# Kernel tuning notes

Measured on AMD Instinct MI355X. Metric: run time of the kernel, lower is better.

## Reference

```python
import jax, jax.numpy as jnp
import numpy as np

B, T, E, H = 2, 2048, 1024, 16
HS = E // H  # head size = 64
EPS = 1e-5


def setup_inputs() -> dict:
    key = jax.random.key(0)
    ks = jax.random.split(key, 12)
    s_e = 1.0 / np.sqrt(E)
    s_4e = 1.0 / np.sqrt(4 * E)
    return {
        "x": jax.random.normal(ks[0], (B, T, E), dtype=jnp.float32),
        # per-head projections (no bias), stacked over heads: [H, E, HS]
        "Wq": jax.random.uniform(ks[1], (H, E, HS), jnp.float32, -s_e, s_e),
        "Wk": jax.random.uniform(ks[2], (H, E, HS), jnp.float32, -s_e, s_e),
        "Wv": jax.random.uniform(ks[3], (H, E, HS), jnp.float32, -s_e, s_e),
        # output projection
        "Wo": jax.random.uniform(ks[4], (E, E), jnp.float32, -s_e, s_e),
        "bo": jax.random.uniform(ks[5], (E,), jnp.float32, -s_e, s_e),
        # feed-forward
        "W1": jax.random.uniform(ks[6], (E, 4 * E), jnp.float32, -s_e, s_e),
        "b1": jax.random.uniform(ks[7], (4 * E,), jnp.float32, -s_e, s_e),
        "W2": jax.random.uniform(ks[8], (4 * E, E), jnp.float32, -s_4e, s_4e),
        "b2": jax.random.uniform(ks[9], (E,), jnp.float32, -s_4e, s_4e),
        # layernorms
        "g1": jnp.ones((E,), jnp.float32),
        "be1": jnp.zeros((E,), jnp.float32),
        "g2": jnp.ones((E,), jnp.float32),
        "be2": jnp.zeros((E,), jnp.float32),
    }


def _layernorm(x, g, b):
    mu = jnp.mean(x, axis=-1, keepdims=True)
    var = jnp.var(x, axis=-1, keepdims=True)
    return (x - mu) * jax.lax.rsqrt(var + EPS) * g + b


def reference(x, Wq, Wk, Wv, Wo, bo, W1, b1, W2, b2, g1, be1, g2, be2):
    Bx, Tx, Ex = x.shape
    # --- multi-head causal self-attention (dropout = identity in eval) ---
    q = jnp.einsum("bte,hed->bhtd", x, Wq)
    k = jnp.einsum("bte,hed->bhtd", x, Wk)
    v = jnp.einsum("bte,hed->bhtd", x, Wv)
    scale = HS ** -0.5
    scores = jnp.einsum("bhtd,bhsd->bhts", q, k) * scale  # [B,H,T,T]
    causal = jnp.tril(jnp.ones((Tx, Tx), dtype=bool))
    scores = jnp.where(causal, scores, -jnp.inf)
    att = jax.nn.softmax(scores, axis=-1)
    out = jnp.einsum("bhts,bhsd->bhtd", att, v)  # [B,H,T,HS]
    out = out.transpose(0, 2, 1, 3).reshape(Bx, Tx, Ex)  # concat heads
    out = out @ Wo + bo
    # --- residual + LN1 ---
    x = _layernorm(x + out, g1, be1)
    # --- feed-forward ---
    h = jax.nn.relu(x @ W1 + b1)
    ff = h @ W2 + b2
    # --- residual + LN2 ---
    return _layernorm(x + ff, g2, be2)
```

## Files before the change

### kernel.cpp

```cpp
#include <hip/hip_runtime.h>
#include <hip/hip_bf16.h>
#include <cstdint>
#include <cstddef>

typedef __hip_bfloat16 bf16;
typedef __attribute__((ext_vector_type(8))) short short8;
typedef __attribute__((ext_vector_type(4))) float f32x4;

#define B_  2
#define T_  2048
#define E_  1024
#define H_  16
#define HS_ 64
#define EPS_ 1e-5f
#define NEG_BIG -1.0e30f
#define SCL2E 0.18033688011112042f

__device__ __forceinline__ float b2f(bf16 v) { return __bfloat162float(v); }
__device__ __forceinline__ bf16  f2b(float v) { return __float2bfloat16(v); }
__device__ __forceinline__ ushort f2bs(float v) { bf16 b = __float2bfloat16(v); return *(ushort*)&b; }
__device__ __forceinline__ float ld1(const bf16* p) { return b2f(*p); }
__device__ __forceinline__ float ld1(const float* p) { return *p; }
__device__ __forceinline__ void st1(bf16* p, float v) { *p = f2b(v); }
__device__ __forceinline__ void st1(float* p, float v) { *p = v; }

__device__ __forceinline__ float fexp2(float x) {
#if __has_builtin(__builtin_amdgcn_exp2f)
    return __builtin_amdgcn_exp2f(x);
#else
    return exp2f(x);
#endif
}

__device__ __forceinline__ void gload16(const void* g, const void* l) {
    __builtin_amdgcn_global_load_lds(
        (const __attribute__((address_space(1))) unsigned int*)(size_t)g,
        (__attribute__((address_space(3))) unsigned int*)(unsigned int)(size_t)l,
        16, 0, 0);
}

__device__ __forceinline__ void transpose_tile_s(short t[64][72],
                                                 const float* in, size_t ldin,
                                                 bf16* out, size_t ldout,
                                                 int r0, int c0)
{
    const int tid = threadIdx.x;
    const int tr = tid >> 2, tc4 = (tid & 3) * 16;

    const float* p = in + (size_t)(r0 + tr) * ldin + c0 + tc4;
    float4 v0 = ((const float4*)p)[0], v1 = ((const float4*)p)[1];
    float4 v2 = ((const float4*)p)[2], v3 = ((const float4*)p)[3];
    union { ushort u[16]; uint4 q[2]; } pk;
    pk.u[0] = f2bs(v0.x); pk.u[1] = f2bs(v0.y); pk.u[2]  = f2bs(v0.z); pk.u[3]  = f2bs(v0.w);
    pk.u[4] = f2bs(v1.x); pk.u[5] = f2bs(v1.y); pk.u[6]  = f2bs(v1.z); pk.u[7]  = f2bs(v1.w);
    pk.u[8] = f2bs(v2.x); pk.u[9] = f2bs(v2.y); pk.u[10] = f2bs(v2.z); pk.u[11] = f2bs(v2.w);
    pk.u[12] = f2bs(v3.x); pk.u[13] = f2bs(v3.y); pk.u[14] = f2bs(v3.z); pk.u[15] = f2bs(v3.w);
    *(uint4*)&t[tr][tc4]     = pk.q[0];
    *(uint4*)&t[tr][tc4 + 8] = pk.q[1];
    __syncthreads();

    const int tcI = tid >> 2, rj = (tid & 3) * 16;
    union { ushort u[16]; uint4 q[2]; } po;
    #pragma unroll
    for (int j = 0; j < 16; j++) po.u[j] = (ushort)t[rj + j][tcI];
    bf16* op = out + (size_t)(c0 + tcI) * ldout + r0 + rj;
    ((uint4*)op)[0] = po.q[0];
    ((uint4*)op)[1] = po.q[1];
}

__global__ __launch_bounds__(256) void prep_kernel(const float* __restrict__ x,
                                                   ushort* __restrict__ xb,
                                                   const float* __restrict__ Wq,
                                                   const float* __restrict__ Wk,
                                                   const float* __restrict__ Wv,
                                                   bf16* __restrict__ WqkvT,
                                                   const float* __restrict__ Wo,
                                                   bf16* __restrict__ WoT)
{
    __shared__ short t[64][72];
    const int bid = blockIdx.x;
    if (bid < 2048) {
        int i = (bid * 256 + (int)threadIdx.x) * 8;
        float4 a = ((const float4*)(x + i))[0];
        float4 b = ((const float4*)(x + i))[1];
        union { ushort u[8]; uint4 v; } p;
        p.u[0] = f2bs(a.x); p.u[1] = f2bs(a.y); p.u[2] = f2bs(a.z); p.u[3] = f2bs(a.w);
        p.u[4] = f2bs(b.x); p.u[5] = f2bs(b.y); p.u[6] = f2bs(b.z); p.u[7] = f2bs(b.w);
        *(uint4*)(xb + i) = p.v;
    } else if (bid < 2048 + 768) {
        const int i = bid - 2048;
        const int s = i >> 4, xt = i & 15;
        const int proj = s >> 4, h = s & 15;
        const float* W = (proj == 0) ? Wq : ((proj == 1) ? Wk : Wv);
        transpose_tile_s(t, W + (size_t)h * E_ * HS_, HS_,
                         WqkvT + ((size_t)proj * E_ + h * 64) * E_, E_,
                         xt * 64, 0);
    } else {
        const int i = bid - 2816;
        transpose_tile_s(t, Wo, E_, WoT, E_, (i >> 4) * 64, (i & 15) * 64);
    }
}

__global__ __launch_bounds__(256) void prep2_kernel(const float* __restrict__ W1,
                                                    bf16* __restrict__ W1T,
                                                    const float* __restrict__ W2,
                                                    bf16* __restrict__ W2T)
{
    __shared__ short t[64][72];
    const int bid = blockIdx.x;
    if (bid < 1024) {
        transpose_tile_s(t, W1, 4 * E_, W1T, E_,
                         (bid & 15) * 64, (bid >> 4) * 64);
    } else {
        const int i = bid - 1024;
        transpose_tile_s(t, W2, E_, W2T, 4 * E_,
                         (i >> 4) * 64, (i & 15) * 64);
    }
}

__global__ __launch_bounds__(256) void vt_transpose(const bf16* __restrict__ qkv,
                                                    bf16* __restrict__ vT)
{
    __shared__ short t[64][72];
    const int tid = threadIdx.x;
    const int bh  = blockIdx.y;
    const int b   = bh >> 4, h = bh & 15;
    const int t0  = blockIdx.x * 64;

    const bf16* in = qkv + ((size_t)b * T_) * (3 * E_) + 2 * E_ + h * 64;
    const int tr = tid >> 2, tc4 = (tid & 3) * 16;
    const bf16* p = in + (size_t)(t0 + tr) * (3 * E_) + tc4;
    uint4 q0 = ((const uint4*)p)[0];
    uint4 q1 = ((const uint4*)p)[1];
    *(uint4*)&t[tr][tc4]     = q0;
    *(uint4*)&t[tr][tc4 + 8] = q1;
    __syncthreads();

    const int tcI = tid >> 2, rj = (tid & 3) * 16;
    union { ushort u[16]; uint4 q[2]; } po;
    #pragma unroll
    for (int j = 0; j < 16; j++) po.u[j] = (ushort)t[rj + j][tcI];
    bf16* op = vT + ((size_t)bh * 64 + tcI) * T_ + t0 + rj;
    ((uint4*)op)[0] = po.q[0];
    ((uint4*)op)[1] = po.q[1];
}

template <int WROWS, int WCOLS, int MF, int NF, int KS, bool BIAS, bool RELU,
          typename TO>
__global__ __launch_bounds__(256) void gemm_bt(const bf16* __restrict__ A,
                                               const bf16* __restrict__ BT,
                                               const float* __restrict__ bias,
                                               TO* __restrict__ C,
                                               int M, int N, int K)
{
    constexpr int BM = WROWS * MF * 16;
    constexpr int BN = WCOLS * NF * 16;
    __shared__ short Asm[KS][BM][32];
    __shared__ short Bsm[KS][BN][32];

    const int tid  = threadIdx.x;
    const int wv   = tid >> 6, lane = tid & 63;
    const int quad = lane >> 4, l16 = lane & 15;
    const int row0 = blockIdx.y * BM, col0 = blockIdx.x * BN;
    const int mr0  = (wv / WCOLS) * MF * 16;
    const int nc0  = (wv % WCOLS) * NF * 16;

    const int sr = tid >> 2, sc = tid & 3;
    const bf16* Ag = A  + (size_t)(row0 + sr) * K + sc * 8;
    const bf16* Bg = BT + (size_t)(col0 + (sr % BN)) * K + sc * 8;

    f32x4 acc[MF][NF];
    #pragma unroll
    for (int i = 0; i < MF; i++)
        #pragma unroll
        for (int j = 0; j < NF; j++) acc[i][j] = (f32x4){0.f, 0.f, 0.f, 0.f};

    for (int kt = 0; kt < K; kt += 32 * KS) {
        __syncthreads();
        #pragma unroll
        for (int g = 0; g < KS; g++) {
            #pragma unroll
            for (int l = 0; l < BM / 64; l++)
                gload16(Ag + g * 32 + (size_t)l * 64 * K, &Asm[g][l * 64 + wv * 16][0]);
            #pragma unroll
            for (int l = 0; l < BN / 64; l++)
                gload16(Bg + g * 32 + (size_t)l * 64 * K, &Bsm[g][l * 64 + wv * 16][0]);
        }
        Ag += 32 * KS; Bg += 32 * KS;
        __syncthreads();

        #pragma unroll
        for (int g = 0; g < KS; g++) {
            short8 af[MF], bfr[NF];
            #pragma unroll
            for (int mf = 0; mf < MF; mf++)
                af[mf] = *(const short8*)&Asm[g][mr0 + mf * 16 + l16][quad * 8];
            #pragma unroll
            for (int nf = 0; nf < NF; nf++)
                bfr[nf] = *(const short8*)&Bsm[g][nc0 + nf * 16 + l16][quad * 8];
            #pragma unroll
            for (int mf = 0; mf < MF; mf++)
                #pragma unroll
                for (int nf = 0; nf < NF; nf++)
                    acc[mf][nf] = __builtin_amdgcn_mfma_f32_16x16x32_bf16(
                        af[mf], bfr[nf], acc[mf][nf], 0, 0, 0);
        }
    }

    #pragma unroll
    for (int nf = 0; nf < NF; nf++) {
        const int col = col0 + nc0 + nf * 16 + l16;
        const float bv = BIAS ? bias[col] : 0.f;
        #pragma unroll
        for (int mf = 0; mf < MF; mf++) {
            #pragma unroll
            for (int r = 0; r < 4; r++) {
                const int row = row0 + mr0 + mf * 16 + quad * 4 + r;
                float v = acc[mf][nf][r] + bv;
                if (RELU) v = fmaxf(v, 0.f);
                st1(&C[(size_t)row * N + col], v);
            }
        }
    }
}

__global__ __launch_bounds__(256) void attn_mfma(const bf16* __restrict__ qkv,
                                                 const bf16* __restrict__ vT,
                                                 bf16* __restrict__ outp)
{
    __shared__ short Klds[128][72];
    __shared__ short Vlds[64][136];
    __shared__ short Plds[4][16][136];

    const int tid  = threadIdx.x;
    const int w    = tid >> 6, lane = tid & 63;
    const int quad = lane >> 4, l16 = lane & 15;

    const int p    = blockIdx.y * 32 + blockIdx.x;
    const int bh   = (p & 7) * 4 + ((p >> 3) & 3);
    const int tile = 31 - (p >> 5);
    const int b    = bh >> 4, h = bh & 15;
    const size_t rowb = (size_t)b * T_ * 3 * E_;
    const int t0    = tile * 64;
    const int qbase = t0 + w * 16;

    const int kkey = tid >> 1, kdh = (tid & 1) * 32;
    const bf16* Kg = qkv + rowb + E_ + h * HS_ + kdh;
    const int vd = tid >> 2, vseg = (tid & 3) * 32;
    const bf16* Vg = vT + ((size_t)bh * 64 + vd) * T_ + vseg;

    short8 vone;
    #pragma unroll
    for (int j = 0; j < 8; j++) vone[j] = (short)0x3F80;

    const bf16* Qp = qkv + rowb + (size_t)(qbase + l16) * (3 * E_) + h * HS_;
    const short8 aq0 = *(const short8*)(Qp + quad * 8);
    const short8 aq1 = *(const short8*)(Qp + 32 + quad * 8);

    f32x4 o[4], o4;
    #pragma unroll
    for (int f = 0; f < 4; f++) o[f] = (f32x4){0.f, 0.f, 0.f, 0.f};
    o4 = (f32x4){0.f, 0.f, 0.f, 0.f};
    float mrow = NEG_BIG;

    for (int kt0 = 0; kt0 <= t0; kt0 += 128) {
        __syncthreads();
        {
            const int kr = (kt0 + kkey < T_) ? kt0 + kkey : T_ - 1;
            const bf16* kp = Kg + (size_t)kr * (3 * E_);
            *(uint4*)&Klds[kkey][kdh]      = ((const uint4*)kp)[0];
            *(uint4*)&Klds[kkey][kdh + 8]  = ((const uint4*)kp)[1];
            *(uint4*)&Klds[kkey][kdh + 16] = ((const uint4*)kp)[2];
            *(uint4*)&Klds[kkey][kdh + 24] = ((const uint4*)kp)[3];
            const bf16* vp = Vg + kt0;
            *(uint4*)&Vlds[vd][vseg]       = ((const uint4*)vp)[0];
            *(uint4*)&Vlds[vd][vseg + 8]   = ((const uint4*)vp)[1];
            *(uint4*)&Vlds[vd][vseg + 16]  = ((const uint4*)vp)[2];
            *(uint4*)&Vlds[vd][vseg + 24]  = ((const uint4*)vp)[3];
        }
        __syncthreads();

        const bool active = (kt0 <= qbase + 15);
        const int nv0 = ((qbase + 15 - kt0) >> 4) + 1;
        const int nvalid = active ? (nv0 < 8 ? nv0 : 8) : 0;

        float ps[8][4];
        #pragma unroll
        for (int c = 0; c < 8; c++) {
            if (c < nvalid) {
                const int kc = kt0 + c * 16;
                const int krow = c * 16 + l16;
                short8 bk0 = *(const short8*)&Klds[krow][quad * 8];
                short8 bk1 = *(const short8*)&Klds[krow][32 + quad * 8];
                f32x4 s = (f32x4){0.f, 0.f, 0.f, 0.f};
                s = __builtin_amdgcn_mfma_f32_16x16x32_bf16(bk0, aq0, s, 0, 0, 0);
                s = __builtin_amdgcn_mfma_f32_16x16x32_bf16(bk1, aq1, s, 0, 0, 0);
                const bool needmask = (kc + 15 > qbase);
                #pragma unroll
                for (int r = 0; r < 4; r++) {
                    float sv = s[r] * SCL2E;
                    if (needmask && (kc + quad * 4 + r > qbase + l16)) sv = NEG_BIG;
                    ps[c][r] = sv;
                }
            }
        }
        if (active) {
            float mx = ps[0][0];
            #pragma unroll
            for (int r = 1; r < 4; r++) mx = fmaxf(mx, ps[0][r]);
            #pragma unroll
            for (int c = 1; c < 8; c++)
                if (c < nvalid)
                    #pragma unroll
                    for (int r = 0; r < 4; r++) mx = fmaxf(mx, ps[c][r]);
            mx = fmaxf(mx, __shfl_xor(mx, 16));
            mx = fmaxf(mx, __shfl_xor(mx, 32));
            const float mnew = fmaxf(mrow, mx);
            const float al = fexp2(mrow - mnew);
            mrow = mnew;

            #pragma unroll
            for (int c = 0; c < 8; c++) {
                uint2 pk; pk.x = 0u; pk.y = 0u;
                if (c < nvalid) {
                    const float e0 = fexp2(ps[c][0] - mnew);
                    const float e1 = fexp2(ps[c][1] - mnew);
                    const float e2 = fexp2(ps[c][2] - mnew);
                    const float e3 = fexp2(ps[c][3] - mnew);
                    pk.x = (uint)f2bs(e0) | ((uint)f2bs(e1) << 16);
                    pk.y = (uint)f2bs(e2) | ((uint)f2bs(e3) << 16);
                }
                *(uint2*)&Plds[w][l16][c * 16 + quad * 4] = pk;
            }

            float alo[4];
            #pragma unroll
            for (int r = 0; r < 4; r++) alo[r] = __shfl(al, quad * 4 + r);
            #pragma unroll
            for (int f = 0; f < 4; f++)
                #pragma unroll
                for (int r = 0; r < 4; r++) o[f][r] *= alo[r];
            #pragma unroll
            for (int r = 0; r < 4; r++) o4[r] *= alo[r];

            #pragma unroll
            for (int kg = 0; kg < 4; kg++) {
                short8 pa = *(const short8*)&Plds[w][l16][kg * 32 + quad * 8];
                #pragma unroll
                for (int f = 0; f < 4; f++) {
                    short8 vb = *(const short8*)&Vlds[f * 16 + l16][kg * 32 + quad * 8];
                    o[f] = __builtin_amdgcn_mfma_f32_16x16x32_bf16(pa, vb, o[f], 0, 0, 0);
                }
                o4 = __builtin_amdgcn_mfma_f32_16x16x32_bf16(pa, vone, o4, 0, 0, 0);
            }
        }
    }

    #pragma unroll
    for (int r = 0; r < 4; r++) {
        const float linv = 1.f / o4[r];
        bf16* op = outp + (size_t)(b * T_ + qbase + quad * 4 + r) * E_ + h * HS_;
        #pragma unroll
        for (int f = 0; f < 4; f++)
            op[f * 16 + l16] = f2b(o[f][r] * linv);
    }
}

template <typename TA, typename TR, typename TO>
__global__ __launch_bounds__(256) void ln_kernel(const TA* a,
                                                 const TR* r,
                                                 const float* g,
                                                 const float* be,
                                                 TO* out)
{
    const int row = blockIdx.x;
    const TA* pa = a + (size_t)row * E_;
    const TR* pr = r + (size_t)row * E_;
    TO* po = out + (size_t)row * E_;

    float v[4];
    float sum = 0.f, sq = 0.f;
    #pragma unroll
    for (int j = 0; j < 4; j++) {
        int c = threadIdx.x + j * 256;
        v[j] = ld1(pa + c) + ld1(pr + c);
        sum += v[j];
        sq  += v[j] * v[j];
    }
    #pragma unroll
    for (int o = 32; o >= 1; o >>= 1) {
        sum += __shfl_xor(sum, o);
        sq  += __shfl_xor(sq, o);
    }
    __shared__ float red[8];
    const int wave = threadIdx.x >> 6, lane = threadIdx.x & 63;
    if (lane == 0) { red[wave] = sum; red[4 + wave] = sq; }
    __syncthreads();
    sum = red[0] + red[1] + red[2] + red[3];
    sq  = red[4] + red[5] + red[6] + red[7];

    const float mu  = sum * (1.f / E_);
    const float var = fmaxf(sq * (1.f / E_) - mu * mu, 0.f);
    const float rs  = rsqrtf(var + EPS_);

    #pragma unroll
    for (int j = 0; j < 4; j++) {
        int c = threadIdx.x + j * 256;
        st1(po + c, (v[j] - mu) * rs * g[c] + be[c]);
    }
}

extern "C" void kernel_launch(void* const* d_in, const int* in_sizes, int n_in,
                              void* d_out, int out_size, void* d_ws, size_t ws_size,
                              hipStream_t stream)
{
    (void)in_sizes; (void)n_in; (void)out_size; (void)ws_size;
    const float* x   = (const float*)d_in[0];
    const float* Wq  = (const float*)d_in[1];
    const float* Wk  = (const float*)d_in[2];
    const float* Wv  = (const float*)d_in[3];
    const float* Wo  = (const float*)d_in[4];
    const float* bo  = (const float*)d_in[5];
    const float* W1  = (const float*)d_in[6];
    const float* b1  = (const float*)d_in[7];
    const float* W2  = (const float*)d_in[8];
    const float* b2  = (const float*)d_in[9];
    const float* g1  = (const float*)d_in[10];
    const float* be1 = (const float*)d_in[11];
    const float* g2  = (const float*)d_in[12];
    const float* be2 = (const float*)d_in[13];

    const int M = B_ * T_;
    char* ws = (char*)d_ws;
    bf16* WqkvT = (bf16*)(ws);
    bf16* qkv   = (bf16*)(ws + (size_t)6291456);
    bf16* WoT   = (bf16*)(ws + (size_t)31457280);
    bf16* W1T   = (bf16*)(ws);
    bf16* W2T   = (bf16*)(ws + (size_t)8388608);
    bf16* proj  = (bf16*)(ws + (size_t)16777216);
    bf16* y     = (bf16*)(ws + (size_t)25165824);
    bf16* ff    = (bf16*)(ws + (size_t)16777216);

    bf16*  xb      = (bf16*)d_out;
    bf16*  vT      = (bf16*)d_out;
    bf16*  attnout = (bf16*)((char*)d_out + (size_t)8388608);
    bf16*  hbuf    = (bf16*)d_out;
    float* outf    = (float*)d_out;

    prep_kernel<<<3072, 256, 0, stream>>>(x, (ushort*)xb, Wq, Wk, Wv, WqkvT, Wo, WoT);

    gemm_bt<2, 2, 4, 4, 2, false, false, bf16><<<dim3(24, 32), 256, 0, stream>>>(
        xb, WqkvT, nullptr, qkv, M, 3 * E_, E_);

    vt_transpose<<<dim3(T_ / 64, B_ * H_), 256, 0, stream>>>(qkv, vT);

    attn_mfma<<<dim3(32, 32), 256, 0, stream>>>(qkv, vT, attnout);

    prep2_kernel<<<2048, 256, 0, stream>>>(W1, W1T, W2, W2T);

    gemm_bt<2, 2, 4, 2, 2, true, false, bf16><<<dim3(16, 32), 256, 0, stream>>>(
        attnout, WoT, bo, proj, M, E_, E_);

    ln_kernel<float, bf16, bf16><<<M, 256, 0, stream>>>(x, proj, g1, be1, y);

    for (int half = 0; half < 2; half++) {
        const size_t r0 = (size_t)half * 2048;
        gemm_bt<2, 2, 4, 4, 2, true, true, bf16><<<dim3(32, 16), 256, 0, stream>>>(
            y + r0 * E_, W1T, b1, hbuf, 2048, 4 * E_, E_);
        gemm_bt<2, 2, 4, 2, 2, true, false, bf16><<<dim3(16, 16), 256, 0, stream>>>(
            hbuf, W2T, b2, ff + r0 * E_, 2048, E_, 4 * E_);
    }

    ln_kernel<bf16, bf16, float><<<M, 256, 0, stream>>>(y, ff, g2, be2, outf);
}
```

Baseline: 422.6 us.

## Split FFN over hidden dimension instead of rows, accumulate second GEMM

The feed-forward block is now split along the 4E hidden dimension instead of the token rows. Each half computes a full-M slice of relu(yW1+b1) into the scratch buffer. The second GEMM uses a strided B operand (new ldb parameter) and a new accumulate-into-output epilogue to sum the two partial products. The W2 GEMM also switches to smaller 64x64 tiles to raise the block count. The aim is to reuse each W1/W2 slice across all rows and improve occupancy, at the cost of a read-modify-write of the output and an intermediate bf16 rounding of the partial sums.

After: 380.8 us. -9.9%, faster.

```diff
diff --git a/kernel.cpp b/kernel.cpp
--- a/kernel.cpp
+++ b/kernel.cpp
@@ -146,12 +146,12 @@
 }
 
 template <int WROWS, int WCOLS, int MF, int NF, int KS, bool BIAS, bool RELU,
-          typename TO>
+          bool ACC, typename TO>
 __global__ __launch_bounds__(256) void gemm_bt(const bf16* __restrict__ A,
                                                const bf16* __restrict__ BT,
                                                const float* __restrict__ bias,
                                                TO* __restrict__ C,
-                                               int M, int N, int K)
+                                               int M, int N, int K, int ldb)
 {
     constexpr int BM = WROWS * MF * 16;
     constexpr int BN = WCOLS * NF * 16;
@@ -167,7 +167,7 @@
 
     const int sr = tid >> 2, sc = tid & 3;
     const bf16* Ag = A  + (size_t)(row0 + sr) * K + sc * 8;
-    const bf16* Bg = BT + (size_t)(col0 + (sr % BN)) * K + sc * 8;
+    const bf16* Bg = BT + (size_t)(col0 + (sr % BN)) * ldb + sc * 8;
 
     f32x4 acc[MF][NF];
     #pragma unroll
@@ -184,7 +184,7 @@
                 gload16(Ag + g * 32 + (size_t)l * 64 * K, &Asm[g][l * 64 + wv * 16][0]);
             #pragma unroll
             for (int l = 0; l < BN / 64; l++)
-                gload16(Bg + g * 32 + (size_t)l * 64 * K, &Bsm[g][l * 64 + wv * 16][0]);
+                gload16(Bg + g * 32 + (size_t)l * 64 * ldb, &Bsm[g][l * 64 + wv * 16][0]);
         }
         Ag += 32 * KS; Bg += 32 * KS;
         __syncthreads();
@@ -217,6 +217,7 @@
             for (int r = 0; r < 4; r++) {
                 const int row = row0 + mr0 + mf * 16 + quad * 4 + r;
                 float v = acc[mf][nf][r] + bv;
+                if (ACC) v += ld1(&C[(size_t)row * N + col]);
                 if (RELU) v = fmaxf(v, 0.f);
                 st1(&C[(size_t)row * N + col], v);
             }
@@ -449,8 +450,8 @@
 
     prep_kernel<<<3072, 256, 0, stream>>>(x, (ushort*)xb, Wq, Wk, Wv, WqkvT, Wo, WoT);
 
-    gemm_bt<2, 2, 4, 4, 2, false, false, bf16><<<dim3(24, 32), 256, 0, stream>>>(
-        xb, WqkvT, nullptr, qkv, M, 3 * E_, E_);
+    gemm_bt<2, 2, 4, 4, 2, false, false, false, bf16><<<dim3(24, 32), 256, 0, stream>>>(
+        xb, WqkvT, nullptr, qkv, M, 3 * E_, E_, E_);
 
     vt_transpose<<<dim3(T_ / 64, B_ * H_), 256, 0, stream>>>(qkv, vT);
 
@@ -458,17 +459,21 @@
 
     prep2_kernel<<<2048, 256, 0, stream>>>(W1, W1T, W2, W2T);
 
-    gemm_bt<2, 2, 4, 2, 2, true, false, bf16><<<dim3(16, 32), 256, 0, stream>>>(
-        attnout, WoT, bo, proj, M, E_, E_);
+    gemm_bt<2, 2, 4, 2, 2, true, false, false, bf16><<<dim3(16, 32), 256, 0, stream>>>(
+        attnout, WoT, bo, proj, M, E_, E_, E_);
 
     ln_kernel<float, bf16, bf16><<<M, 256, 0, stream>>>(x, proj, g1, be1, y);
 
     for (int half = 0; half < 2; half++) {
-        const size_t r0 = (size_t)half * 2048;
-        gemm_bt<2, 2, 4, 4, 2, true, true, bf16><<<dim3(32, 16), 256, 0, stream>>>(
-            y + r0 * E_, W1T, b1, hbuf, 2048, 4 * E_, E_);
-        gemm_bt<2, 2, 4, 2, 2, true, false, bf16><<<dim3(16, 16), 256, 0, stream>>>(
-            hbuf, W2T, b2, ff + r0 * E_, 2048, E_, 4 * E_);
+        const size_t c0 = (size_t)half * 2048;
+        gemm_bt<2, 2, 4, 4, 2, true, true, false, bf16><<<dim3(16, 32), 256, 0, stream>>>(
+            y, W1T + c0 * E_, b1 + c0, hbuf, M, 2048, E_, E_);
+        if (half == 0)
+            gemm_bt<2, 2, 2, 2, 2, true, false, false, bf16><<<dim3(16, 64), 256, 0, stream>>>(
+                hbuf, W2T + c0, b2, ff, M, E_, 2048, 4 * E_);
+        else
+            gemm_bt<2, 2, 2, 2, 2, false, false, true, bf16><<<dim3(16, 64), 256, 0, stream>>>(
+                hbuf, W2T + c0, nullptr, ff, M, E_, 2048, 4 * E_);
     }
 
     ln_kernel<bf16, bf16, float><<<M, 256, 0, stream>>>(y, ff, g2, be2, outf);
```
